# Kernel optimization log

Measured on AMD Instinct MI355X. Metric: run time of the kernel, lower is better.

Reference implementation:

```python
import jax, jax.numpy as jnp
import numpy as np

N_NODES = 50000
N_EDGES = 800000
IN_C, HID_C, OUT_C = 128, 128, 1


def setup_inputs() -> dict:
    key = jax.random.key(0)
    ks = jax.random.split(key, 10)
    x = jax.random.normal(ks[0], (N_NODES, IN_C), dtype=jnp.float32)
    x2 = jax.random.normal(ks[1], (1,), dtype=jnp.float32)
    edge_index = jax.random.randint(ks[2], (2, N_EDGES), 0, N_NODES, dtype=jnp.int64)
    # GCNConv params (glorot-ish scale) and final linear
    W1 = jax.random.normal(ks[3], (IN_C, HID_C), dtype=jnp.float32) / np.sqrt(IN_C)
    b1 = jnp.zeros((HID_C,), dtype=jnp.float32)
    W2 = jax.random.normal(ks[4], (HID_C, HID_C), dtype=jnp.float32) / np.sqrt(HID_C)
    b2 = jnp.zeros((HID_C,), dtype=jnp.float32)
    Wlin = jax.random.normal(ks[5], (HID_C, OUT_C), dtype=jnp.float32) / np.sqrt(HID_C)
    blin = jnp.zeros((OUT_C,), dtype=jnp.float32)
    return {"x": x, "x2": x2, "edge_index": edge_index, "num_nodes": N_NODES,
            "W1": W1, "b1": b1, "W2": W2, "b2": b2, "Wlin": Wlin, "blin": blin}


def _gcn_conv(h, W, b, src, dst, norm, num_nodes):
    # linear transform then normalized scatter-add aggregation (PyG GCNConv)
    h = h @ W  # [N, C_out]
    msg = h[src] * norm[:, None]  # gather + scale, [E+N, C_out]
    out = jax.ops.segment_sum(msg, dst, num_segments=num_nodes)
    return out + b


def _gcn_norm(edge_index, num_nodes):
    # add self-loops, compute sym-normalization coefficients D^-1/2 A D^-1/2
    loop = jnp.arange(num_nodes, dtype=edge_index.dtype)
    src = jnp.concatenate([edge_index[0], loop])
    dst = jnp.concatenate([edge_index[1], loop])
    ones = jnp.ones(src.shape[0], dtype=jnp.float32)
    deg = jax.ops.segment_sum(ones, dst, num_segments=num_nodes)
    dinv = jnp.where(deg > 0, jax.lax.rsqrt(deg), 0.0)
    norm = dinv[src] * dinv[dst]
    return src, dst, norm


def reference(x, x2, edge_index, num_nodes, W1, b1, W2, b2, Wlin, blin):
    src, dst, norm = _gcn_norm(edge_index, num_nodes)
    h = _gcn_conv(x, W1, b1, src, dst, norm, num_nodes)
    h = jax.nn.relu(h)
    # dropout is identity in eval mode
    h = _gcn_conv(h, W2, b2, src, dst, norm, num_nodes)
    h = jax.nn.relu(h)
    out = h @ Wlin + blin  # [N, 1]
    return out.squeeze(-1)
```

## Files before the change

kernel.cpp:

```cpp
#include <hip/hip_runtime.h>
#include <hip/hip_bf16.h>

#define N_NODES 50000
#define N_EDGES 800000
#define C 128

#define NBB   391
#define CAPB  2600
#define CHUNK 2048

typedef __attribute__((ext_vector_type(8))) short short8v;
typedef __attribute__((ext_vector_type(4))) float f32x4;

__global__ __launch_bounds__(256) void k_binA(const int* __restrict__ ei,
                                              int* __restrict__ gcur,
                                              int2* __restrict__ tmp) {
    __shared__ int hist[NBB];
    __shared__ int lbase[NBB];
    __shared__ int gbaseL[NBB];
    __shared__ int stmp[256];
    __shared__ int2 buf[CHUNK];
    __shared__ int totalv;

    int tid = threadIdx.x;
    int e0 = blockIdx.x * CHUNK;

    for (int i = tid; i < NBB; i += 256) hist[i] = 0;
    __syncthreads();

    int sarr[8], darr[8], parr[8];
#pragma unroll
    for (int j = 0; j < 8; ++j) {
        int e = e0 + j * 256 + tid;
        darr[j] = -1;
        if (e < N_EDGES) {
            sarr[j] = ei[e];
            int d = ei[N_EDGES + e];
            darr[j] = d;
            parr[j] = atomicAdd(&hist[d >> 7], 1);
        }
    }
    __syncthreads();

    {
        int i0 = 2 * tid, i1 = 2 * tid + 1;
        int c0 = (i0 < NBB) ? hist[i0] : 0;
        int c1 = (i1 < NBB) ? hist[i1] : 0;
        int c = c0 + c1;
        stmp[tid] = c;
        __syncthreads();
        int v = c;
        for (int d = 1; d < 256; d <<= 1) {
            int w = (tid >= d) ? stmp[tid - d] : 0;
            __syncthreads();
            v += w;
            stmp[tid] = v;
            __syncthreads();
        }
        int excl = v - c;
        if (i0 < NBB) lbase[i0] = excl;
        if (i1 < NBB) lbase[i1] = excl + c0;
        if (tid == 255) totalv = v;
    }
    for (int i = tid; i < NBB; i += 256) {
        int cnt = hist[i];
        int run = (cnt > 0) ? atomicAdd(&gcur[i], cnt) : 0;
        gbaseL[i] = i * CAPB + run;
    }
    __syncthreads();

#pragma unroll
    for (int j = 0; j < 8; ++j) {
        if (darr[j] >= 0) {
            int b = darr[j] >> 7;
            buf[lbase[b] + parr[j]] = make_int2(sarr[j], darr[j]);
        }
    }
    __syncthreads();

    int total = totalv;
    for (int i = tid; i < total; i += 256) {
        int2 v = buf[i];
        int b = v.y >> 7;
        int gpos = gbaseL[b] + (i - lbase[b]);
        if (gpos < (b + 1) * CAPB) tmp[gpos] = v;
    }
}

__global__ __launch_bounds__(256) void k_dinv(const int2* __restrict__ tmp,
                                              const int* __restrict__ gcur,
                                              float* __restrict__ dinv) {
    __shared__ int cnt[128];
    int b = blockIdx.x, tid = threadIdx.x;
    if (tid < 128) cnt[tid] = 0;
    __syncthreads();
    int n = gcur[b];
    if (n > CAPB) n = CAPB;
    for (int i = tid; i < n; i += 256)
        atomicAdd(&cnt[tmp[b * CAPB + i].y & 127], 1);
    __syncthreads();
    int node = b * 128 + tid;
    if (tid < 128 && node < N_NODES)
        dinv[node] = rsqrtf((float)cnt[tid] + 1.0f);
}

__device__ __forceinline__ unsigned int bf16rtn(float f) {
    unsigned int u = __float_as_uint(f);
    return (u + 0x7fffu + ((u >> 16) & 1u)) >> 16;
}
__device__ __forceinline__ unsigned int packbf2(float lo, float hi) {
    return bf16rtn(lo) | (bf16rtn(hi) << 16);
}

__global__ void k_prepW(const float* __restrict__ W1, const float* __restrict__ W2,
                        unsigned short* __restrict__ Wsplit) {
    int t = blockIdx.x * 256 + threadIdx.x;
    if (t >= 32768) return;
    int layer = t >> 14, idx = t & 16383;
    int i = idx >> 7, j = idx & 127;
    const float* Wsrc = layer ? W2 : W1;
    float w = Wsrc[i * 128 + j];
    unsigned int h = bf16rtn(w);
    float hf = __uint_as_float(h << 16);
    unsigned int l = bf16rtn(w - hf);
    unsigned short* base = Wsplit + layer * 32768;
    base[j * 128 + i] = (unsigned short)h;
    base[16384 + j * 128 + i] = (unsigned short)l;
}

template <bool RELU>
__global__ __launch_bounds__(512, 4) void k_gemm(const float* __restrict__ A,
                                                 const unsigned short* __restrict__ Whg,
                                                 const unsigned short* __restrict__ Wlg,
                                                 const float* __restrict__ dinv,
                                                 unsigned short* __restrict__ Hout) {
    __shared__ uint4 Al[64 * 16];
    __shared__ float ddv[64];

    int tid = threadIdx.x;
    int row0 = blockIdx.x * 64;
    int wv = tid >> 6, lane = tid & 63;
    int col = wv * 16 + (lane & 15);
    int kq = lane >> 4;

    const uint4* Bh4 = (const uint4*)Whg;
    const uint4* Bl4 = (const uint4*)Wlg;
    short8v bh[4], bl[4];
#pragma unroll
    for (int ks = 0; ks < 4; ++ks) {
        uint4 uh = Bh4[col * 16 + ks * 4 + kq];
        uint4 ul = Bl4[col * 16 + ks * 4 + kq];
        bh[ks] = *reinterpret_cast<short8v*>(&uh);
        bl[ks] = *reinterpret_cast<short8v*>(&ul);
    }

#pragma unroll
    for (int pass = 0; pass < 2; ++pass) {
        int row = (tid >> 4) + pass * 32;
        int o = tid & 15;
        int gr = row0 + row;
        float4 v0 = make_float4(0.f, 0.f, 0.f, 0.f), v1 = v0;
        if (gr < N_NODES) {
            const float4* A4 = (const float4*)A;
            v0 = A4[gr * 32 + o * 2];
            v1 = A4[gr * 32 + o * 2 + 1];
        }
        if (RELU) {
            v0.x = fmaxf(v0.x, 0.f); v0.y = fmaxf(v0.y, 0.f);
            v0.z = fmaxf(v0.z, 0.f); v0.w = fmaxf(v0.w, 0.f);
            v1.x = fmaxf(v1.x, 0.f); v1.y = fmaxf(v1.y, 0.f);
            v1.z = fmaxf(v1.z, 0.f); v1.w = fmaxf(v1.w, 0.f);
        }
        uint4 u;
        u.x = packbf2(v0.x, v0.y);
        u.y = packbf2(v0.z, v0.w);
        u.z = packbf2(v1.x, v1.y);
        u.w = packbf2(v1.z, v1.w);
        int byte = (row * 256 + o * 16) ^ ((row & 7) << 4);
        Al[byte >> 4] = u;
    }
    if (tid < 64) {
        int gr = row0 + tid;
        ddv[tid] = (gr < N_NODES) ? dinv[gr] : 0.f;
    }
    __syncthreads();

    f32x4 acc[4];
#pragma unroll
    for (int st = 0; st < 4; ++st) acc[st] = (f32x4){0.f, 0.f, 0.f, 0.f};

#pragma unroll
    for (int st = 0; st < 4; ++st) {
        int rowl = st * 16 + (lane & 15);
        int rbase = rowl * 256;
        int swz = (rowl & 7) << 4;
#pragma unroll
        for (int ks = 0; ks < 4; ++ks) {
            int byte = (rbase + ks * 64 + kq * 16) ^ swz;
            uint4 ua = Al[byte >> 4];
            short8v a = *reinterpret_cast<short8v*>(&ua);
            acc[st] = __builtin_amdgcn_mfma_f32_16x16x32_bf16(a, bh[ks], acc[st], 0, 0, 0);
            acc[st] = __builtin_amdgcn_mfma_f32_16x16x32_bf16(a, bl[ks], acc[st], 0, 0, 0);
        }
    }

#pragma unroll
    for (int st = 0; st < 4; ++st) {
#pragma unroll
        for (int r = 0; r < 4; ++r) {
            int rowl = st * 16 + kq * 4 + r;
            int gr = row0 + rowl;
            if (gr < N_NODES) {
                float dv = ddv[rowl];
                Hout[gr * 128 + col] = (unsigned short)bf16rtn(dv * acc[st][r]);
            }
        }
    }
}

__device__ __forceinline__ void add8(float* acc, uint4 u) {
    acc[0] += __uint_as_float(u.x << 16);
    acc[1] += __uint_as_float(u.x & 0xffff0000u);
    acc[2] += __uint_as_float(u.y << 16);
    acc[3] += __uint_as_float(u.y & 0xffff0000u);
    acc[4] += __uint_as_float(u.z << 16);
    acc[5] += __uint_as_float(u.z & 0xffff0000u);
    acc[6] += __uint_as_float(u.w << 16);
    acc[7] += __uint_as_float(u.w & 0xffff0000u);
}

template <bool FINAL>
__global__ __launch_bounds__(1024) void k_agg(const uint4* __restrict__ h4,
                                              const int2* __restrict__ tmp,
                                              const int* __restrict__ gcur,
                                              const float* __restrict__ bias,
                                              const float* __restrict__ Wlin,
                                              const float* __restrict__ blin,
                                              float* __restrict__ aggout) {
    __shared__ int   rawsrc[CAPB];
    __shared__ short rawloc[CAPB];
    __shared__ int   lcsr[CAPB];
    __shared__ int   lcnt[128];
    __shared__ int   lbase0[128];
    __shared__ int   lcur[128];
    __shared__ int   stmp[128];

    int b = blockIdx.x, tid = threadIdx.x;
    int cnt = gcur[b];
    if (cnt > CAPB) cnt = CAPB;

    if (tid < 128) { lcnt[tid] = 0; lcur[tid] = 0; }
    __syncthreads();

    for (int i = tid; i < cnt; i += 1024) {
        int2 v = tmp[b * CAPB + i];
        int l = v.y & 127;
        rawsrc[i] = v.x;
        rawloc[i] = (short)l;
        atomicAdd(&lcnt[l], 1);
    }
    __syncthreads();

    {
        int c = (tid < 128) ? lcnt[tid] : 0;
        if (tid < 128) stmp[tid] = c;
        __syncthreads();
        int v = c;
        for (int d = 1; d < 128; d <<= 1) {
            int w = (tid >= d && tid < 128) ? stmp[tid - d] : 0;
            __syncthreads();
            if (tid < 128) { v += w; stmp[tid] = v; }
            __syncthreads();
        }
        if (tid < 128) lbase0[tid] = v - c;
    }
    __syncthreads();

    for (int i = tid; i < cnt; i += 1024) {
        int l = rawloc[i];
        int p = atomicAdd(&lcur[l], 1);
        lcsr[lbase0[l] + p] = rawsrc[i];
    }
    __syncthreads();

    int wv = tid >> 6, lane = tid & 63, eg = lane >> 4, cq = lane & 15;

    float4 bv0 = ((const float4*)bias)[cq * 2];
    float4 bv1 = ((const float4*)bias)[cq * 2 + 1];
    float4 wl0 = make_float4(0.f, 0.f, 0.f, 0.f), wl1 = wl0;
    float bl = 0.f;
    if (FINAL) {
        wl0 = ((const float4*)Wlin)[cq * 2];
        wl1 = ((const float4*)Wlin)[cq * 2 + 1];
        bl = blin[0];
    }

#pragma unroll 1
    for (int t = 0; t < 8; ++t) {
        int ln = wv * 8 + t;
        int node = b * 128 + ln;
        if (node >= N_NODES) break;
        int deg = lcnt[ln];
        int o0 = lbase0[ln], o1 = o0 + deg;

        float acc[8];
#pragma unroll
        for (int j = 0; j < 8; ++j) acc[j] = 0.f;

        int e = o0;
        for (; e + 8 <= o1; e += 8) {
            int s0 = lcsr[e + 2 * eg];
            int s1 = lcsr[e + 2 * eg + 1];
            uint4 u0 = h4[s0 * 16 + cq];
            uint4 u1 = h4[s1 * 16 + cq];
            add8(acc, u0);
            add8(acc, u1);
        }
        {
            int r = o1 - e;
            int b0 = e + 2 * eg;
            if (2 * eg < r)     { int s = lcsr[b0];     add8(acc, h4[s * 16 + cq]); }
            if (2 * eg + 1 < r) { int s = lcsr[b0 + 1]; add8(acc, h4[s * 16 + cq]); }
        }
#pragma unroll
        for (int j = 0; j < 8; ++j) {
            acc[j] += __shfl_xor(acc[j], 16, 64);
            acc[j] += __shfl_xor(acc[j], 32, 64);
        }

        float dv = rsqrtf((float)deg + 1.0f);
        uint4 us = h4[node * 16 + cq];
        float hv[8];
        hv[0] = __uint_as_float(us.x << 16); hv[1] = __uint_as_float(us.x & 0xffff0000u);
        hv[2] = __uint_as_float(us.y << 16); hv[3] = __uint_as_float(us.y & 0xffff0000u);
        hv[4] = __uint_as_float(us.z << 16); hv[5] = __uint_as_float(us.z & 0xffff0000u);
        hv[6] = __uint_as_float(us.w << 16); hv[7] = __uint_as_float(us.w & 0xffff0000u);
        float o[8];
        o[0] = dv * (acc[0] + hv[0]) + bv0.x;
        o[1] = dv * (acc[1] + hv[1]) + bv0.y;
        o[2] = dv * (acc[2] + hv[2]) + bv0.z;
        o[3] = dv * (acc[3] + hv[3]) + bv0.w;
        o[4] = dv * (acc[4] + hv[4]) + bv1.x;
        o[5] = dv * (acc[5] + hv[5]) + bv1.y;
        o[6] = dv * (acc[6] + hv[6]) + bv1.z;
        o[7] = dv * (acc[7] + hv[7]) + bv1.w;

        if (!FINAL) {
            if (eg == 0) {
                float4* out4 = (float4*)aggout;
                out4[node * 32 + cq * 2]     = make_float4(o[0], o[1], o[2], o[3]);
                out4[node * 32 + cq * 2 + 1] = make_float4(o[4], o[5], o[6], o[7]);
            }
        } else {
            float v = fmaxf(o[0], 0.f) * wl0.x + fmaxf(o[1], 0.f) * wl0.y
                    + fmaxf(o[2], 0.f) * wl0.z + fmaxf(o[3], 0.f) * wl0.w
                    + fmaxf(o[4], 0.f) * wl1.x + fmaxf(o[5], 0.f) * wl1.y
                    + fmaxf(o[6], 0.f) * wl1.z + fmaxf(o[7], 0.f) * wl1.w;
            v += __shfl_xor(v, 1, 64);
            v += __shfl_xor(v, 2, 64);
            v += __shfl_xor(v, 4, 64);
            v += __shfl_xor(v, 8, 64);
            if (lane == 0) aggout[node] = v + bl;
        }
    }
}

extern "C" void kernel_launch(void* const* d_in, const int* in_sizes, int n_in,
                              void* d_out, int out_size, void* d_ws, size_t ws_size,
                              hipStream_t stream) {
    const float* x    = (const float*)d_in[0];
    const int*   ei   = (const int*)d_in[2];
    const float* W1   = (const float*)d_in[4];
    const float* b1   = (const float*)d_in[5];
    const float* W2   = (const float*)d_in[6];
    const float* b2   = (const float*)d_in[7];
    const float* Wlin = (const float*)d_in[8];
    const float* blin = (const float*)d_in[9];
    float* out = (float*)d_out;

    char* ws = (char*)d_ws;
    size_t off = 0;
    auto carve = [&](size_t bytes) -> void* {
        void* p = ws + off;
        off = (off + bytes + 255) & ~(size_t)255;
        return p;
    };
    int*   gcur = (int*)  carve(NBB * sizeof(int));
    float* dinv = (float*)carve(N_NODES * sizeof(float));
    int2*  tmp  = (int2*) carve((size_t)NBB * CAPB * sizeof(int2));
    unsigned short* hbf = (unsigned short*)carve((size_t)N_NODES * C * sizeof(unsigned short));
    float* agg  = (float*)carve((size_t)N_NODES * C * sizeof(float));
    unsigned short* wsplit = (unsigned short*)carve(4 * 16384 * sizeof(unsigned short));

    const int NB_A = (N_EDGES + CHUNK - 1) / CHUNK;
    const int NB_G = (N_NODES + 63) / 64;

    hipMemsetAsync(gcur, 0, NBB * sizeof(int), stream);

    k_prepW<<<128, 256, 0, stream>>>(W1, W2, wsplit);
    k_binA<<<NB_A, 256, 0, stream>>>(ei, gcur, tmp);
    k_dinv<<<NBB, 256, 0, stream>>>(tmp, gcur, dinv);

    const unsigned short* W1h = wsplit;
    const unsigned short* W1l = wsplit + 16384;
    const unsigned short* W2h = wsplit + 32768;
    const unsigned short* W2l = wsplit + 49152;

    k_gemm<false><<<NB_G, 512, 0, stream>>>(x, W1h, W1l, dinv, hbf);
    k_agg<false><<<NBB, 1024, 0, stream>>>((const uint4*)hbf, tmp, gcur,
                                           b1, Wlin, blin, agg);
    k_gemm<true><<<NB_G, 512, 0, stream>>>(agg, W2h, W2l, dinv, hbf);
    k_agg<true><<<NBB, 1024, 0, stream>>>((const uint4*)hbf, tmp, gcur,
                                          b2, Wlin, blin, out);
}
```

Before: 202.0 us.

## Store layer-1 output as bf16 with fused ReLU, split aggregation blocks in half

The first aggregation now applies ReLU and writes bf16 instead of fp32, so the second GEMM reads half the bytes and skips the conversion. Each aggregation bucket is split across two 512-thread blocks, each handling 64 nodes, for more blocks and better occupancy. Prefix scans now use wavefront shuffles instead of shared-memory barriers, the gather is unrolled to four loads per lane, and the memset is folded into k_prepW. The cost is that each bucket's edge list is read twice.

Measured after the change: 217.9 us. 1.08x slower.

```diff
diff --git a/kernel.cpp b/kernel.cpp
--- a/kernel.cpp
+++ b/kernel.cpp
@@ -12,98 +12,6 @@
 typedef __attribute__((ext_vector_type(8))) short short8v;
 typedef __attribute__((ext_vector_type(4))) float f32x4;
 
-__global__ __launch_bounds__(256) void k_binA(const int* __restrict__ ei,
-                                              int* __restrict__ gcur,
-                                              int2* __restrict__ tmp) {
-    __shared__ int hist[NBB];
-    __shared__ int lbase[NBB];
-    __shared__ int gbaseL[NBB];
-    __shared__ int stmp[256];
-    __shared__ int2 buf[CHUNK];
-    __shared__ int totalv;
-
-    int tid = threadIdx.x;
-    int e0 = blockIdx.x * CHUNK;
-
-    for (int i = tid; i < NBB; i += 256) hist[i] = 0;
-    __syncthreads();
-
-    int sarr[8], darr[8], parr[8];
-#pragma unroll
-    for (int j = 0; j < 8; ++j) {
-        int e = e0 + j * 256 + tid;
-        darr[j] = -1;
-        if (e < N_EDGES) {
-            sarr[j] = ei[e];
-            int d = ei[N_EDGES + e];
-            darr[j] = d;
-            parr[j] = atomicAdd(&hist[d >> 7], 1);
-        }
-    }
-    __syncthreads();
-
-    {
-        int i0 = 2 * tid, i1 = 2 * tid + 1;
-        int c0 = (i0 < NBB) ? hist[i0] : 0;
-        int c1 = (i1 < NBB) ? hist[i1] : 0;
-        int c = c0 + c1;
-        stmp[tid] = c;
-        __syncthreads();
-        int v = c;
-        for (int d = 1; d < 256; d <<= 1) {
-            int w = (tid >= d) ? stmp[tid - d] : 0;
-            __syncthreads();
-            v += w;
-            stmp[tid] = v;
-            __syncthreads();
-        }
-        int excl = v - c;
-        if (i0 < NBB) lbase[i0] = excl;
-        if (i1 < NBB) lbase[i1] = excl + c0;
-        if (tid == 255) totalv = v;
-    }
-    for (int i = tid; i < NBB; i += 256) {
-        int cnt = hist[i];
-        int run = (cnt > 0) ? atomicAdd(&gcur[i], cnt) : 0;
-        gbaseL[i] = i * CAPB + run;
-    }
-    __syncthreads();
-
-#pragma unroll
-    for (int j = 0; j < 8; ++j) {
-        if (darr[j] >= 0) {
-            int b = darr[j] >> 7;
-            buf[lbase[b] + parr[j]] = make_int2(sarr[j], darr[j]);
-        }
-    }
-    __syncthreads();
-
-    int total = totalv;
-    for (int i = tid; i < total; i += 256) {
-        int2 v = buf[i];
-        int b = v.y >> 7;
-        int gpos = gbaseL[b] + (i - lbase[b]);
-        if (gpos < (b + 1) * CAPB) tmp[gpos] = v;
-    }
-}
-
-__global__ __launch_bounds__(256) void k_dinv(const int2* __restrict__ tmp,
-                                              const int* __restrict__ gcur,
-                                              float* __restrict__ dinv) {
-    __shared__ int cnt[128];
-    int b = blockIdx.x, tid = threadIdx.x;
-    if (tid < 128) cnt[tid] = 0;
-    __syncthreads();
-    int n = gcur[b];
-    if (n > CAPB) n = CAPB;
-    for (int i = tid; i < n; i += 256)
-        atomicAdd(&cnt[tmp[b * CAPB + i].y & 127], 1);
-    __syncthreads();
-    int node = b * 128 + tid;
-    if (tid < 128 && node < N_NODES)
-        dinv[node] = rsqrtf((float)cnt[tid] + 1.0f);
-}
-
 __device__ __forceinline__ unsigned int bf16rtn(float f) {
     unsigned int u = __float_as_uint(f);
     return (u + 0x7fffu + ((u >> 16) & 1u)) >> 16;
@@ -113,8 +21,9 @@
 }
 
 __global__ void k_prepW(const float* __restrict__ W1, const float* __restrict__ W2,
-                        unsigned short* __restrict__ Wsplit) {
+                        unsigned short* __restrict__ Wsplit, int* __restrict__ gcur) {
     int t = blockIdx.x * 256 + threadIdx.x;
+    if (t < NBB) gcur[t] = 0;
     if (t >= 32768) return;
     int layer = t >> 14, idx = t & 16383;
     int i = idx >> 7, j = idx & 127;
@@ -128,8 +37,102 @@
     base[16384 + j * 128 + i] = (unsigned short)l;
 }
 
-template <bool RELU>
-__global__ __launch_bounds__(512, 4) void k_gemm(const float* __restrict__ A,
+__global__ __launch_bounds__(256) void k_binA(const int* __restrict__ ei,
+                                              int* __restrict__ gcur,
+                                              int2* __restrict__ tmp) {
+    __shared__ int hist[NBB];
+    __shared__ int lbase[NBB];
+    __shared__ int gbaseL[NBB];
+    __shared__ int wsum[4];
+    __shared__ int2 buf[CHUNK];
+    __shared__ int totalv;
+
+    int tid = threadIdx.x;
+    int e0 = blockIdx.x * CHUNK;
+
+    for (int i = tid; i < NBB; i += 256) hist[i] = 0;
+    __syncthreads();
+
+    int sarr[8], darr[8], parr[8];
+#pragma unroll
+    for (int j = 0; j < 8; ++j) {
+        int e = e0 + j * 256 + tid;
+        darr[j] = -1;
+        if (e < N_EDGES) {
+            sarr[j] = ei[e];
+            int d = ei[N_EDGES + e];
+            darr[j] = d;
+            parr[j] = atomicAdd(&hist[d >> 7], 1);
+        }
+    }
+    __syncthreads();
+
+    {
+        int i0 = 2 * tid, i1 = i0 + 1;
+        int c0 = (i0 < NBB) ? hist[i0] : 0;
+        int c1 = (i1 < NBB) ? hist[i1] : 0;
+        int c = c0 + c1;
+        int lane = tid & 63, w = tid >> 6;
+        int s = c;
+#pragma unroll
+        for (int d = 1; d < 64; d <<= 1) {
+            int u = __shfl_up(s, d, 64);
+            if (lane >= d) s += u;
+        }
+        if (lane == 63) wsum[w] = s;
+        __syncthreads();
+        int add = 0;
+        for (int i = 0; i < w; ++i) add += wsum[i];
+        int incl = s + add;
+        int excl = incl - c;
+        if (i0 < NBB) lbase[i0] = excl;
+        if (i1 < NBB) lbase[i1] = excl + c0;
+        if (tid == 255) totalv = incl;
+    }
+    for (int i = tid; i < NBB; i += 256) {
+        int cnt = hist[i];
+        int run = (cnt > 0) ? atomicAdd(&gcur[i], cnt) : 0;
+        gbaseL[i] = i * CAPB + run;
+    }
+    __syncthreads();
+
+#pragma unroll
+    for (int j = 0; j < 8; ++j) {
+        if (darr[j] >= 0) {
+            int b = darr[j] >> 7;
+            buf[lbase[b] + parr[j]] = make_int2(sarr[j], darr[j]);
+        }
+    }
+    __syncthreads();
+
+    int total = totalv;
+    for (int i = tid; i < total; i += 256) {
+        int2 v = buf[i];
+        int b = v.y >> 7;
+        int gpos = gbaseL[b] + (i - lbase[b]);
+        if (gpos < (b + 1) * CAPB) tmp[gpos] = v;
+    }
+}
+
+__global__ __launch_bounds__(256) void k_dinv(const int2* __restrict__ tmp,
+                                              const int* __restrict__ gcur,
+                                              float* __restrict__ dinv) {
+    __shared__ int cnt[128];
+    int b = blockIdx.x, tid = threadIdx.x;
+    if (tid < 128) cnt[tid] = 0;
+    __syncthreads();
+    int n = gcur[b];
+    if (n > CAPB) n = CAPB;
+    for (int i = tid; i < n; i += 256)
+        atomicAdd(&cnt[tmp[b * CAPB + i].y & 127], 1);
+    __syncthreads();
+    int node = b * 128 + tid;
+    if (tid < 128 && node < N_NODES)
+        dinv[node] = rsqrtf((float)cnt[tid] + 1.0f);
+}
+
+template <bool AF32>
+__global__ __launch_bounds__(512, 4) void k_gemm(const void* __restrict__ Ain,
                                                  const unsigned short* __restrict__ Whg,
                                                  const unsigned short* __restrict__ Wlg,
                                                  const float* __restrict__ dinv,
@@ -159,23 +162,21 @@
         int row = (tid >> 4) + pass * 32;
         int o = tid & 15;
         int gr = row0 + row;
-        float4 v0 = make_float4(0.f, 0.f, 0.f, 0.f), v1 = v0;
-        if (gr < N_NODES) {
-            const float4* A4 = (const float4*)A;
-            v0 = A4[gr * 32 + o * 2];
-            v1 = A4[gr * 32 + o * 2 + 1];
-        }
-        if (RELU) {
-            v0.x = fmaxf(v0.x, 0.f); v0.y = fmaxf(v0.y, 0.f);
-            v0.z = fmaxf(v0.z, 0.f); v0.w = fmaxf(v0.w, 0.f);
-            v1.x = fmaxf(v1.x, 0.f); v1.y = fmaxf(v1.y, 0.f);
-            v1.z = fmaxf(v1.z, 0.f); v1.w = fmaxf(v1.w, 0.f);
-        }
-        uint4 u;
-        u.x = packbf2(v0.x, v0.y);
-        u.y = packbf2(v0.z, v0.w);
-        u.z = packbf2(v1.x, v1.y);
-        u.w = packbf2(v1.z, v1.w);
+        uint4 u = make_uint4(0u, 0u, 0u, 0u);
+        if (AF32) {
+            float4 v0 = make_float4(0.f, 0.f, 0.f, 0.f), v1 = v0;
+            if (gr < N_NODES) {
+                const float4* A4 = (const float4*)Ain;
+                v0 = A4[gr * 32 + o * 2];
+                v1 = A4[gr * 32 + o * 2 + 1];
+            }
+            u.x = packbf2(v0.x, v0.y);
+            u.y = packbf2(v0.z, v0.w);
+            u.z = packbf2(v1.x, v1.y);
+            u.w = packbf2(v1.z, v1.w);
+        } else {
+            if (gr < N_NODES) u = ((const uint4*)Ain)[gr * 16 + o];
+        }
         int byte = (row * 256 + o * 16) ^ ((row & 7) << 4);
         Al[byte >> 4] = u;
     }
@@ -230,56 +231,58 @@
 }
 
 template <bool FINAL>
-__global__ __launch_bounds__(1024) void k_agg(const uint4* __restrict__ h4,
-                                              const int2* __restrict__ tmp,
-                                              const int* __restrict__ gcur,
-                                              const float* __restrict__ bias,
-                                              const float* __restrict__ Wlin,
-                                              const float* __restrict__ blin,
-                                              float* __restrict__ aggout) {
+__global__ __launch_bounds__(512, 6) void k_agg(const uint4* __restrict__ h4,
+                                                const int2* __restrict__ tmp,
+                                                const int* __restrict__ gcur,
+                                                const float* __restrict__ bias,
+                                                const float* __restrict__ Wlin,
+                                                const float* __restrict__ blin,
+                                                void* __restrict__ aggout) {
     __shared__ int   rawsrc[CAPB];
     __shared__ short rawloc[CAPB];
     __shared__ int   lcsr[CAPB];
-    __shared__ int   lcnt[128];
-    __shared__ int   lbase0[128];
-    __shared__ int   lcur[128];
-    __shared__ int   stmp[128];
-
-    int b = blockIdx.x, tid = threadIdx.x;
+    __shared__ int   lcnt[64];
+    __shared__ int   lbase0[64];
+    __shared__ int   lcur[64];
+
+    int blk = blockIdx.x;
+    int b = blk >> 1, half = blk & 1;
+    int tid = threadIdx.x;
     int cnt = gcur[b];
     if (cnt > CAPB) cnt = CAPB;
 
-    if (tid < 128) { lcnt[tid] = 0; lcur[tid] = 0; }
-    __syncthreads();
-
-    for (int i = tid; i < cnt; i += 1024) {
-        int2 v = tmp[b * CAPB + i];
+    if (tid < 64) { lcnt[tid] = 0; lcur[tid] = 0; }
+    __syncthreads();
+
+    const int2* tmpb = tmp + (size_t)b * CAPB;
+    for (int i = tid; i < cnt; i += 512) {
+        int2 v = tmpb[i];
         int l = v.y & 127;
         rawsrc[i] = v.x;
         rawloc[i] = (short)l;
-        atomicAdd(&lcnt[l], 1);
-    }
-    __syncthreads();
-
-    {
-        int c = (tid < 128) ? lcnt[tid] : 0;
-        if (tid < 128) stmp[tid] = c;
-        __syncthreads();
-        int v = c;
-        for (int d = 1; d < 128; d <<= 1) {
-            int w = (tid >= d && tid < 128) ? stmp[tid - d] : 0;
-            __syncthreads();
-            if (tid < 128) { v += w; stmp[tid] = v; }
-            __syncthreads();
-        }
-        if (tid < 128) lbase0[tid] = v - c;
-    }
-    __syncthreads();
-
-    for (int i = tid; i < cnt; i += 1024) {
+        if ((l >> 6) == half) atomicAdd(&lcnt[l & 63], 1);
+    }
+    __syncthreads();
+
+    if (tid < 64) {
+        int c = lcnt[tid];
+        int s = c;
+#pragma unroll
+        for (int d = 1; d < 64; d <<= 1) {
+            int u = __shfl_up(s, d, 64);
+            if (tid >= d) s += u;
+        }
+        lbase0[tid] = s - c;
+    }
+    __syncthreads();
+
+    for (int i = tid; i < cnt; i += 512) {
         int l = rawloc[i];
-        int p = atomicAdd(&lcur[l], 1);
-        lcsr[lbase0[l] + p] = rawsrc[i];
+        if ((l >> 6) == half) {
+            int ll = l & 63;
+            int p = atomicAdd(&lcur[ll], 1);
+            lcsr[lbase0[ll] + p] = rawsrc[i];
+        }
     }
     __syncthreads();
 
@@ -297,30 +300,41 @@
 
 #pragma unroll 1
     for (int t = 0; t < 8; ++t) {
-        int ln = wv * 8 + t;
-        int node = b * 128 + ln;
+        int ll = wv * 8 + t;
+        int node = b * 128 + half * 64 + ll;
         if (node >= N_NODES) break;
-        int deg = lcnt[ln];
-        int o0 = lbase0[ln], o1 = o0 + deg;
+        int deg = lcnt[ll];
+        int o0 = lbase0[ll], o1 = o0 + deg;
+
+        uint4 us = h4[node * 16 + cq];
 
         float acc[8];
 #pragma unroll
         for (int j = 0; j < 8; ++j) acc[j] = 0.f;
 
         int e = o0;
-        for (; e + 8 <= o1; e += 8) {
-            int s0 = lcsr[e + 2 * eg];
-            int s1 = lcsr[e + 2 * eg + 1];
+        for (; e + 16 <= o1; e += 16) {
+            int b0 = e + 4 * eg;
+            int s0 = lcsr[b0], s1 = lcsr[b0 + 1], s2 = lcsr[b0 + 2], s3 = lcsr[b0 + 3];
             uint4 u0 = h4[s0 * 16 + cq];
             uint4 u1 = h4[s1 * 16 + cq];
-            add8(acc, u0);
-            add8(acc, u1);
+            uint4 u2 = h4[s2 * 16 + cq];
+            uint4 u3 = h4[s3 * 16 + cq];
+            add8(acc, u0); add8(acc, u1); add8(acc, u2); add8(acc, u3);
+        }
+        if (e + 8 <= o1) {
+            int b0 = e + 2 * eg;
+            int s0 = lcsr[b0], s1 = lcsr[b0 + 1];
+            uint4 u0 = h4[s0 * 16 + cq];
+            uint4 u1 = h4[s1 * 16 + cq];
+            add8(acc, u0); add8(acc, u1);
+            e += 8;
         }
         {
             int r = o1 - e;
             int b0 = e + 2 * eg;
-            if (2 * eg < r)     { int s = lcsr[b0];     add8(acc, h4[s * 16 + cq]); }
-            if (2 * eg + 1 < r) { int s = lcsr[b0 + 1]; add8(acc, h4[s * 16 + cq]); }
+            if (2 * eg < r)     add8(acc, h4[lcsr[b0] * 16 + cq]);
+            if (2 * eg + 1 < r) add8(acc, h4[lcsr[b0 + 1] * 16 + cq]);
         }
 #pragma unroll
         for (int j = 0; j < 8; ++j) {
@@ -329,7 +343,6 @@
         }
 
         float dv = rsqrtf((float)deg + 1.0f);
-        uint4 us = h4[node * 16 + cq];
         float hv[8];
         hv[0] = __uint_as_float(us.x << 16); hv[1] = __uint_as_float(us.x & 0xffff0000u);
         hv[2] = __uint_as_float(us.y << 16); hv[3] = __uint_as_float(us.y & 0xffff0000u);
@@ -347,9 +360,12 @@
 
         if (!FINAL) {
             if (eg == 0) {
-                float4* out4 = (float4*)aggout;
-                out4[node * 32 + cq * 2]     = make_float4(o[0], o[1], o[2], o[3]);
-                out4[node * 32 + cq * 2 + 1] = make_float4(o[4], o[5], o[6], o[7]);
+                uint4 u;
+                u.x = packbf2(fmaxf(o[0], 0.f), fmaxf(o[1], 0.f));
+                u.y = packbf2(fmaxf(o[2], 0.f), fmaxf(o[3], 0.f));
+                u.z = packbf2(fmaxf(o[4], 0.f), fmaxf(o[5], 0.f));
+                u.w = packbf2(fmaxf(o[6], 0.f), fmaxf(o[7], 0.f));
+                ((uint4*)aggout)[node * 16 + cq] = u;
             }
         } else {
             float v = fmaxf(o[0], 0.f) * wl0.x + fmaxf(o[1], 0.f) * wl0.y
@@ -360,7 +376,7 @@
             v += __shfl_xor(v, 2, 64);
             v += __shfl_xor(v, 4, 64);
             v += __shfl_xor(v, 8, 64);
-            if (lane == 0) aggout[node] = v + bl;
+            if (lane == 0) ((float*)aggout)[node] = v + bl;
         }
     }
 }
@@ -388,28 +404,27 @@
     int*   gcur = (int*)  carve(NBB * sizeof(int));
     float* dinv = (float*)carve(N_NODES * sizeof(float));
     int2*  tmp  = (int2*) carve((size_t)NBB * CAPB * sizeof(int2));
-    unsigned short* hbf = (unsigned short*)carve((size_t)N_NODES * C * sizeof(unsigned short));
-    float* agg  = (float*)carve((size_t)N_NODES * C * sizeof(float));
+    unsigned short* hbf  = (unsigned short*)carve((size_t)N_NODES * C * sizeof(unsigned short));
+    unsigned short* hbf2 = (unsigned short*)carve((size_t)N_NODES * C * sizeof(unsigned short));
     unsigned short* wsplit = (unsigned short*)carve(4 * 16384 * sizeof(unsigned short));
 
     const int NB_A = (N_EDGES + CHUNK - 1) / CHUNK;
     const int NB_G = (N_NODES + 63) / 64;
-
-    hipMemsetAsync(gcur, 0, NBB * sizeof(int), stream);
-
-    k_prepW<<<128, 256, 0, stream>>>(W1, W2, wsplit);
-    k_binA<<<NB_A, 256, 0, stream>>>(ei, gcur, tmp);
-    k_dinv<<<NBB, 256, 0, stream>>>(tmp, gcur, dinv);
+    const int NB_H = 2 * NBB;
 
     const unsigned short* W1h = wsplit;
     const unsigned short* W1l = wsplit + 16384;
     const unsigned short* W2h = wsplit + 32768;
     const unsigned short* W2l = wsplit + 49152;
 
-    k_gemm<false><<<NB_G, 512, 0, stream>>>(x, W1h, W1l, dinv, hbf);
-    k_agg<false><<<NBB, 1024, 0, stream>>>((const uint4*)hbf, tmp, gcur,
-                                           b1, Wlin, blin, agg);
-    k_gemm<true><<<NB_G, 512, 0, stream>>>(agg, W2h, W2l, dinv, hbf);
-    k_agg<true><<<NBB, 1024, 0, stream>>>((const uint4*)hbf, tmp, gcur,
+    k_prepW<<<128, 256, 0, stream>>>(W1, W2, wsplit, gcur);
+    k_binA<<<NB_A, 256, 0, stream>>>(ei, gcur, tmp);
+    k_dinv<<<NBB, 256, 0, stream>>>(tmp, gcur, dinv);
+
+    k_gemm<true><<<NB_G, 512, 0, stream>>>(x, W1h, W1l, dinv, hbf);
+    k_agg<false><<<NB_H, 512, 0, stream>>>((const uint4*)hbf, tmp, gcur,
+                                           b1, Wlin, blin, hbf2);
+    k_gemm<false><<<NB_G, 512, 0, stream>>>(hbf2, W2h, W2l, dinv, hbf);
+    k_agg<true><<<NB_H, 512, 0, stream>>>((const uint4*)hbf, tmp, gcur,
                                           b2, Wlin, blin, out);
 }
```
